# Optimization experiments

Measured on AMD Instinct MI355X. Metric: run time of the kernel, lower is better.

## Reference

```python
import jax, jax.numpy as jnp
import numpy as np

B, S, C = 4, 2048, 1024
H, D = 16, 64            # num_heads, head_size
N_STATE = H * D          # 1024
WINDOW = 256             # window_size (causal local window)
SCALE_INV = 1.0 / np.sqrt(D).astype(np.float32)  # sqrt_scale_inv**2 = 1/scale


def setup_inputs() -> dict:
    key = jax.random.key(0)
    ks = jax.random.split(key, 5)
    return {
        "x": jax.random.normal(ks[0], (B, S, C), dtype=jnp.float32),
        "W_qkv": jax.random.normal(ks[1], (3 * N_STATE, C), dtype=jnp.float32) * 0.02,
        "b_qkv": jax.random.normal(ks[2], (3 * N_STATE,), dtype=jnp.float32) * 0.02,
        "W_proj": jax.random.normal(ks[3], (C, N_STATE), dtype=jnp.float32) * 0.02,
        "b_proj": jax.random.normal(ks[4], (C,), dtype=jnp.float32) * 0.02,
    }


def reference(x, W_qkv, b_qkv, W_proj, b_proj):
    # fused QKV projection (channel_last Linear: y = x @ W.T + b)
    qkv = jnp.einsum("bsc,nc->bsn", x, W_qkv) + b_qkv        # [B,S,3*n_state]
    q, k, v = jnp.split(qkv, 3, axis=-1)

    def split_heads(t):  # [B,S,H*D] -> [B,H,S,D]
        return t.reshape(B, S, H, D).transpose(0, 2, 1, 3)

    q, k, v = split_heads(q), split_heads(k), split_heads(v)

    # scaled dot scores: matmul then multiply by 1/scale (scale = sqrt(head_size))
    scores = jnp.einsum("bhqd,bhkd->bhqk", q, k) * SCALE_INV  # [B,H,S,S]

    # window_ar mask: key j visible to query i iff 0 <= i - j < WINDOW
    i = jnp.arange(S)[:, None]
    j = jnp.arange(S)[None, :]
    allowed = (j <= i) & (i - j < WINDOW)                     # [S,S]
    scores = jnp.where(allowed, scores, -jnp.inf)

    attn = jax.nn.softmax(scores, axis=-1)                    # [B,H,S,S]
    ctx = jnp.einsum("bhqk,bhkd->bhqd", attn, v)              # [B,H,S,D]
    ctx = ctx.transpose(0, 2, 1, 3).reshape(B, S, N_STATE)    # merge heads

    out = jnp.einsum("bsn,cn->bsc", ctx, W_proj) + b_proj     # [B,S,C]
    return out
```

## Files before the change

kernel.cpp:

```cpp
#include <hip/hip_runtime.h>
#include <stdint.h>

#define S_LEN 2048
#define NH 16
#define HD 64
#define CDIM 1024
#define QKV_LD 3072
#define WIN 256

typedef __attribute__((ext_vector_type(8))) short bf16x8;
typedef __attribute__((ext_vector_type(4))) short bf16x4;
typedef __attribute__((ext_vector_type(4))) float f32x4;

__device__ __forceinline__ short f2bf(float f) {
  uint32_t u = __builtin_bit_cast(uint32_t, f);
  u += 0x7fffu + ((u >> 16) & 1u);
  return (short)(u >> 16);
}

__global__ void cvt_f32_bf16(const float* __restrict__ in, short* __restrict__ out, int n4) {
  int i = blockIdx.x * 256 + threadIdx.x;
  if (i >= n4) return;
  float4 v = ((const float4*)in)[i];
  bf16x4 o;
  o[0] = f2bf(v.x); o[1] = f2bf(v.y); o[2] = f2bf(v.z); o[3] = f2bf(v.w);
  ((bf16x4*)out)[i] = o;
}

__device__ __forceinline__ void gl_lds16(const short* g, short* lds) {
  __builtin_amdgcn_global_load_lds(
      (const __attribute__((address_space(1))) uint32_t*)(uintptr_t)g,
      (__attribute__((address_space(3))) uint32_t*)(uintptr_t)lds,
      16, 0, 0);
}

#define WAITVM(N) asm volatile("s_waitcnt vmcnt(" #N ")" ::: "memory")

template <int BF16OUT>
__global__ __launch_bounds__(512) void gemm_ring(
    const short* __restrict__ A, const short* __restrict__ Bt,
    const float* __restrict__ bias, void* __restrict__ Cout, int N)
{
  constexpr int K = 1024;
  constexpr int NSUB = 32;
  __shared__ __align__(16) short Asm[4][128 * 32];
  __shared__ __align__(16) short Bsm[4][256 * 32];
  const int tid = threadIdx.x, wave = tid >> 6, lane = tid & 63;
  const int wm = wave >> 2, wn = wave & 3;
  const int cl = lane & 15, g = lane >> 4;

  const int gx = gridDim.x;
  const int nwg = gx * gridDim.y;
  const int flat = blockIdx.y * gx + blockIdx.x;
  const int swzb = (flat & 7) * (nwg >> 3) + (flat >> 3);
  const int m0 = (swzb / gx) * 128;
  const int n0 = (swzb % gx) * 256;

  const int srow = tid >> 2;
  const int scol = (((tid & 3) ^ ((tid >> 3) & 3)) << 3);
  const short* Asrc  = A  + (size_t)(m0 + srow) * K + scol;
  const short* Bsrc0 = Bt + (size_t)(n0 + srow) * K + scol;
  const short* Bsrc1 = Bt + (size_t)(n0 + 128 + srow) * K + scol;
  const int ldso = tid * 8;

  auto stage = [&](int j) {
    const int st = j & 3;
    gl_lds16(Asrc  + j * 32, &Asm[st][ldso]);
    gl_lds16(Bsrc0 + j * 32, &Bsm[st][ldso]);
    gl_lds16(Bsrc1 + j * 32, &Bsm[st][4096 + ldso]);
  };

  const int rc = (g ^ ((cl >> 1) & 3)) << 3;
  const int arow = wm * 64 + cl;
  const int brow = wn * 64 + cl;

  f32x4 acc[4][4] = {};
  bf16x8 a0[4], b0[4], a1[4], b1[4];

  stage(0); stage(1); stage(2);
  WAITVM(3);
  __builtin_amdgcn_s_barrier();

#define READF(AA, BB, jj) { const int _s = (jj) & 3;                          \
  _Pragma("unroll") for (int i = 0; i < 4; i++)                               \
    AA[i] = *(const bf16x8*)&Asm[_s][(arow + i * 16) * 32 + rc];              \
  _Pragma("unroll") for (int n = 0; n < 4; n++)                               \
    BB[n] = *(const bf16x8*)&Bsm[_s][(brow + n * 16) * 32 + rc]; }

#define MFMA16(AA, BB)                                                        \
  __builtin_amdgcn_s_setprio(1);                                              \
  _Pragma("unroll") for (int i = 0; i < 4; i++)                               \
    _Pragma("unroll") for (int n = 0; n < 4; n++)                             \
      acc[i][n] = __builtin_amdgcn_mfma_f32_16x16x32_bf16(AA[i], BB[n], acc[i][n], 0, 0, 0); \
  __builtin_amdgcn_s_setprio(0);

  READF(a0, b0, 0);
  for (int j = 0; j < NSUB; j += 2) {
    READF(a1, b1, j + 1);
    if (j + 3 < NSUB) { stage(j + 3); WAITVM(3); } else { WAITVM(0); }
    __builtin_amdgcn_s_barrier();
    MFMA16(a0, b0);

    if (j + 2 < NSUB) READF(a0, b0, j + 2);
    if (j + 4 < NSUB) { stage(j + 4); WAITVM(3); } else { WAITVM(0); }
    __builtin_amdgcn_s_barrier();
    MFMA16(a1, b1);
  }
#undef READF
#undef MFMA16

#pragma unroll
  for (int n = 0; n < 4; n++) {
    const int col = n0 + wn * 64 + n * 16 + cl;
    const float bs = bias[col];
#pragma unroll
    for (int i = 0; i < 4; i++) {
      const int row = m0 + wm * 64 + i * 16 + g * 4;
#pragma unroll
      for (int e = 0; e < 4; e++) {
        const float v = acc[i][n][e] + bs;
        if (BF16OUT) ((short*)Cout)[(size_t)(row + e) * N + col] = f2bf(v);
        else         ((float*)Cout)[(size_t)(row + e) * N + col] = v;
      }
    }
  }
}

__global__ __launch_bounds__(256) void attn_win(
    const short* __restrict__ qkv, short* __restrict__ ctx)
{
  const int tid = threadIdx.x;
  const int wave = tid >> 6, lane = tid & 63;
  const int grp = blockIdx.x % 32;
  const int h = (blockIdx.x / 32) % NH;
  const int b = blockIdx.x / (32 * NH);
  const int qb = (grp * 4 + wave) * 16;

  const int cl = lane & 15;
  const int g  = lane >> 4;

  const size_t rowQ = (size_t)(b * S_LEN + qb + cl) * QKV_LD + h * HD;
  bf16x8 qf0 = *(const bf16x8*)&qkv[rowQ + g * 8];
  bf16x8 qf1 = *(const bf16x8*)&qkv[rowQ + 32 + g * 8];

  float m_run = -1e30f, l_run = 0.f;
  f32x4 acc[4] = {};
  const f32x4 zero = {};

  const int kstart = qb >= WIN ? qb - WIN : 0;
  const int q_glob = qb + cl;

  for (int k0 = kstart; k0 <= qb; k0 += 16) {
    const size_t rowK = (size_t)(b * S_LEN + k0 + cl) * QKV_LD + CDIM + h * HD;
    bf16x8 kf0 = *(const bf16x8*)&qkv[rowK + g * 8];
    bf16x8 kf1 = *(const bf16x8*)&qkv[rowK + 32 + g * 8];
    f32x4 st = __builtin_amdgcn_mfma_f32_16x16x32_bf16(kf0, qf0, zero, 0, 0, 0);
    st = __builtin_amdgcn_mfma_f32_16x16x32_bf16(kf1, qf1, st, 0, 0, 0);

    float s[4]; bool ok[4];
    float mt = -1e30f;
#pragma unroll
    for (int e = 0; e < 4; e++) {
      int key = k0 + 4 * g + e;
      ok[e] = (key <= q_glob) && (q_glob - key < WIN);
      s[e] = st[e] * 0.125f;
      if (ok[e]) mt = fmaxf(mt, s[e]);
    }
    mt = fmaxf(mt, __shfl_xor(mt, 16, 64));
    mt = fmaxf(mt, __shfl_xor(mt, 32, 64));
    float m_new = fmaxf(m_run, mt);
    float scale = __expf(m_run - m_new);
    float p[4]; float ls = 0.f;
#pragma unroll
    for (int e = 0; e < 4; e++) {
      p[e] = ok[e] ? __expf(s[e] - m_new) : 0.f;
      ls += p[e];
    }
    ls += __shfl_xor(ls, 16, 64);
    ls += __shfl_xor(ls, 32, 64);
    l_run = l_run * scale + ls;
    m_run = m_new;
#pragma unroll
    for (int c = 0; c < 4; c++) acc[c] *= scale;

    bf16x4 pf;
#pragma unroll
    for (int e = 0; e < 4; e++) pf[e] = f2bf(p[e]);

    const size_t rowV = (size_t)(b * S_LEN + k0 + 4 * g) * QKV_LD + 2 * CDIM + h * HD + cl;
#pragma unroll
    for (int c = 0; c < 4; c++) {
      bf16x4 vf;
#pragma unroll
      for (int e = 0; e < 4; e++)
        vf[e] = qkv[rowV + (size_t)e * QKV_LD + c * 16];
      acc[c] = __builtin_amdgcn_mfma_f32_16x16x16bf16_1k(vf, pf, acc[c], 0, 0, 0);
    }
  }

  const float inv_l = 1.f / l_run;
  const size_t rowO = (size_t)(b * S_LEN + qb + cl) * CDIM + h * HD;
#pragma unroll
  for (int c = 0; c < 4; c++)
#pragma unroll
    for (int j = 0; j < 4; j++)
      ctx[rowO + c * 16 + 4 * g + j] = f2bf(acc[c][j] * inv_l);
}

extern "C" void kernel_launch(void* const* d_in, const int* in_sizes, int n_in,
                              void* d_out, int out_size, void* d_ws, size_t ws_size,
                              hipStream_t stream) {
  const float* x      = (const float*)d_in[0];
  const float* W_qkv  = (const float*)d_in[1];
  const float* b_qkv  = (const float*)d_in[2];
  const float* W_proj = (const float*)d_in[3];
  const float* b_proj = (const float*)d_in[4];
  float* out = (float*)d_out;

  const int BS = 4 * S_LEN;
  char* ws = (char*)d_ws;
  short* qkv_bf = (short*)ws;
  short* x_bf   = (short*)(ws + (size_t)BS * QKV_LD * 2);
  short* wq_bf  = x_bf + (size_t)BS * CDIM;
  short* wp_bf  = wq_bf + (size_t)QKV_LD * CDIM;
  short* ctx_bf = wp_bf + (size_t)CDIM * CDIM;

  int n4 = BS * CDIM / 4;
  cvt_f32_bf16<<<(n4 + 255) / 256, 256, 0, stream>>>(x, x_bf, n4);
  n4 = QKV_LD * CDIM / 4;
  cvt_f32_bf16<<<(n4 + 255) / 256, 256, 0, stream>>>(W_qkv, wq_bf, n4);
  n4 = CDIM * CDIM / 4;
  cvt_f32_bf16<<<(n4 + 255) / 256, 256, 0, stream>>>(W_proj, wp_bf, n4);

  dim3 g1(QKV_LD / 256, BS / 128);
  gemm_ring<1><<<g1, 512, 0, stream>>>(x_bf, wq_bf, b_qkv, qkv_bf, QKV_LD);

  attn_win<<<4 * NH * 32, 256, 0, stream>>>(qkv_bf, ctx_bf);

  dim3 g2(CDIM / 256, BS / 128);
  gemm_ring<0><<<g2, 512, 0, stream>>>(ctx_bf, wp_bf, b_proj, out, CDIM);
}
```

Before: 249.9 us.

## Use larger 256x384 tile GEMM with 12 waves for the QKV projection

Adds a dedicated QKV GEMM kernel using 256x384 output tiles, 768 threads and one block per CU, giving exactly 256 workgroups, one per CU on mi355x. Each wave computes a 128x64 sub-tile and splits A reads into low and high halves so LDS reads and global-to-LDS staging interleave with MFMA work. The aim is more operand reuse per LDS load and no partial second wave of blocks. In exchange it uses much more LDS, has higher register pressure from 32 accumulators per lane, and relies on hand-tuned per-wave vmcnt waits.

```diff
diff --git a/kernel.cpp b/kernel.cpp
--- a/kernel.cpp
+++ b/kernel.cpp
@@ -35,6 +35,104 @@
 }
 
 #define WAITVM(N) asm volatile("s_waitcnt vmcnt(" #N ")" ::: "memory")
+
+__global__ __launch_bounds__(768, 1) void gemm_big(
+    const short* __restrict__ A, const short* __restrict__ Bt,
+    const float* __restrict__ bias, short* __restrict__ Cout)
+{
+  constexpr int K = 1024, NSUB = 32, NN = 3072;
+  __shared__ __align__(16) short Asm[4][256 * 32];
+  __shared__ __align__(16) short Bsm[4][384 * 32];
+  const int tid = threadIdx.x, wave = tid >> 6, lane = tid & 63;
+  const int wm = wave / 6, wn = wave % 6;
+  const int cl = lane & 15, g = lane >> 4;
+
+  const int bid = blockIdx.x;
+  const int swzb = (bid & 7) * 32 + (bid >> 3);
+  const int m0 = (swzb & 31) * 256;
+  const int n0 = (swzb >> 5) * 384;
+
+  const int srow = tid >> 2;
+  const int scc = (((tid & 3) ^ ((tid >> 3) & 3)) << 3);
+  const short* aS0 = A  + (size_t)(m0 + srow) * K + scc;
+  const short* aS1 = A  + (size_t)(m0 + 192 + srow) * K + scc;
+  const short* bS0 = Bt + (size_t)(n0 + srow) * K + scc;
+  const short* bS1 = Bt + (size_t)(n0 + 192 + srow) * K + scc;
+  const int d0 = tid * 8, d1 = 6144 + tid * 8;
+
+  auto stA = [&](int t) { const int s = t & 3;
+    gl_lds16(aS0 + t * 32, &Asm[s][d0]);
+    if (tid < 256) gl_lds16(aS1 + t * 32, &Asm[s][d1]);
+  };
+  auto stB = [&](int t) { const int s = t & 3;
+    gl_lds16(bS0 + t * 32, &Bsm[s][d0]);
+    gl_lds16(bS1 + t * 32, &Bsm[s][d1]);
+  };
+
+  const int rc = (g ^ ((cl >> 1) & 3)) << 3;
+  const int arow = wm * 128 + cl;
+  const int brow = wn * 64 + cl;
+
+  bf16x8 aLo[4], aHi[4], b0v[4], b1v[4];
+  f32x4 acc[8][4] = {};
+
+#define RD_ALO(jj) if ((jj) < NSUB) { const int _s = (jj) & 3;                \
+  _Pragma("unroll") for (int i = 0; i < 4; i++)                               \
+    aLo[i] = *(const bf16x8*)&Asm[_s][(arow + i * 16) * 32 + rc]; }
+#define RD_AHI(jj) { const int _s = (jj) & 3;                                 \
+  _Pragma("unroll") for (int i = 0; i < 4; i++)                               \
+    aHi[i] = *(const bf16x8*)&Asm[_s][(arow + 64 + i * 16) * 32 + rc]; }
+#define RD_B(BB, jj) if ((jj) < NSUB) { const int _s = (jj) & 3;              \
+  _Pragma("unroll") for (int n = 0; n < 4; n++)                               \
+    BB[n] = *(const bf16x8*)&Bsm[_s][(brow + n * 16) * 32 + rc]; }
+#define MFMAH(base, AA, BB)                                                   \
+  __builtin_amdgcn_s_setprio(1);                                              \
+  _Pragma("unroll") for (int i = 0; i < 4; i++)                               \
+    _Pragma("unroll") for (int n = 0; n < 4; n++)                             \
+      acc[(base) + i][n] = __builtin_amdgcn_mfma_f32_16x16x32_bf16(           \
+          AA[i], BB[n], acc[(base) + i][n], 0, 0, 0);                         \
+  __builtin_amdgcn_s_setprio(0);
+#define WAITG() { if (wave < 4) { WAITVM(6); } else { WAITVM(4); } }
+
+#define SUBP(jj, BC, BNx)                                                     \
+  RD_AHI(jj);                                                                 \
+  if ((jj) + 3 < NSUB) { stA((jj) + 3); WAITG(); } else { WAITVM(0); }        \
+  __builtin_amdgcn_s_barrier();                                               \
+  MFMAH(0, aLo, BC);                                                          \
+  RD_ALO((jj) + 1); RD_B(BNx, (jj) + 1);                                      \
+  if ((jj) + 3 < NSUB) { stB((jj) + 3); WAITG(); } else { WAITVM(0); }        \
+  __builtin_amdgcn_s_barrier();                                               \
+  MFMAH(4, aHi, BC);
+
+  stA(0); stB(0); stA(1); stB(1); stA(2); stB(2);
+  if (wave < 4) { WAITVM(8); } else { WAITVM(6); }
+  __builtin_amdgcn_s_barrier();
+  RD_ALO(0); RD_B(b0v, 0);
+
+  for (int j = 0; j < NSUB; j += 2) {
+    SUBP(j, b0v, b1v);
+    SUBP(j + 1, b1v, b0v);
+  }
+#undef RD_ALO
+#undef RD_AHI
+#undef RD_B
+#undef MFMAH
+#undef WAITG
+#undef SUBP
+
+#pragma unroll
+  for (int n = 0; n < 4; n++) {
+    const int col = n0 + wn * 64 + n * 16 + cl;
+    const float bs = bias[col];
+#pragma unroll
+    for (int i = 0; i < 8; i++) {
+      const int row = m0 + wm * 128 + i * 16 + g * 4;
+#pragma unroll
+      for (int e = 0; e < 4; e++)
+        Cout[(size_t)(row + e) * NN + col] = f2bf(acc[i][n][e] + bs);
+    }
+  }
+}
 
 template <int BF16OUT>
 __global__ __launch_bounds__(512) void gemm_ring(
@@ -58,7 +156,7 @@
 
   const int srow = tid >> 2;
   const int scol = (((tid & 3) ^ ((tid >> 3) & 3)) << 3);
-  const short* Asrc  = A  + (size_t)(m0 + srow) * K + scol;
+  const short* Asrc  = A + (size_t)(m0 + srow) * K + scol;
   const short* Bsrc0 = Bt + (size_t)(n0 + srow) * K + scol;
   const short* Bsrc1 = Bt + (size_t)(n0 + 128 + srow) * K + scol;
   const int ldso = tid * 8;
@@ -232,8 +330,7 @@
   n4 = CDIM * CDIM / 4;
   cvt_f32_bf16<<<(n4 + 255) / 256, 256, 0, stream>>>(W_proj, wp_bf, n4);
 
-  dim3 g1(QKV_LD / 256, BS / 128);
-  gemm_ring<1><<<g1, 512, 0, stream>>>(x_bf, wq_bf, b_qkv, qkv_bf, QKV_LD);
+  gemm_big<<<256, 768, 0, stream>>>(x_bf, wq_bf, b_qkv, qkv_bf);
 
   attn_win<<<4 * NH * 32, 256, 0, stream>>>(qkv_bf, ctx_bf);
 
```

Result: slower. 601.8 us (+140.9%).

## Replace QKV GEMM with 256x384-tile, 12-wave kernel sized to one wave of CUs

Applied to the files above, without the earlier changes.

Adds a dedicated QKV projection GEMM that uses 256x384 output tiles with 768 threads (12 waves, each computing 128x64). The grid is exactly 256 workgroups, matching the CU count, which removes the tail effect of the previous 768-block launch and raises arithmetic intensity per LDS load. A and B staging are split across the two half-steps, and explicit lgkmcnt waits and sched barriers are added around the MFMA phases. The cost is lower occupancy (one block per CU with large LDS and register use) and extra barriers per k-step, which may expose latency.

```diff
diff --git a/kernel.cpp b/kernel.cpp
--- a/kernel.cpp
+++ b/kernel.cpp
@@ -35,6 +35,110 @@
 }
 
 #define WAITVM(N) asm volatile("s_waitcnt vmcnt(" #N ")" ::: "memory")
+
+__global__ __launch_bounds__(768, 1) void gemm_qkv(
+    const short* __restrict__ A, const short* __restrict__ Bt,
+    const float* __restrict__ bias, short* __restrict__ Cout)
+{
+  constexpr int K = 1024, NSUB = 32, NN = 3072;
+  __shared__ __align__(16) short Asm[4][256 * 32];
+  __shared__ __align__(16) short Bsm[4][384 * 32];
+  const int tid = threadIdx.x, wave = tid >> 6, lane = tid & 63;
+  const int wm = wave / 6, wn = wave % 6;
+  const int cl = lane & 15, g = lane >> 4;
+
+  const int bid = blockIdx.x;
+  const int swzb = (bid & 7) * 32 + (bid >> 3);
+  const int m0 = (swzb & 31) * 256;
+  const int n0 = (swzb >> 5) * 384;
+
+  const int srow = tid >> 2;
+  const int scc = (((tid & 3) ^ ((tid >> 3) & 3)) << 3);
+  const short* aS0 = A  + (size_t)(m0 + srow) * K + scc;
+  const short* aS1 = A  + (size_t)(m0 + 128 + srow) * K + scc;
+  const short* bS0 = Bt + (size_t)(n0 + srow) * K + scc;
+  const short* bS1 = Bt + (size_t)(n0 + 192 + srow) * K + scc;
+  const int d8 = tid * 8;
+
+  auto stageA = [&](int t) { const int s = t & 3;
+    if (tid < 512) {
+      gl_lds16(aS0 + t * 32, &Asm[s][d8]);
+      gl_lds16(aS1 + t * 32, &Asm[s][4096 + d8]);
+    }
+  };
+  auto stageB = [&](int t) { const int s = t & 3;
+    gl_lds16(bS0 + t * 32, &Bsm[s][d8]);
+    gl_lds16(bS1 + t * 32, &Bsm[s][6144 + d8]);
+  };
+
+  const int rc = (g ^ ((cl >> 1) & 3)) << 3;
+  const int arow = wm * 128 + cl;
+  const int brow = wn * 64 + cl;
+
+  f32x4 acc[8][4] = {};
+
+  stageA(0); stageB(0); stageA(1); stageB(1); stageA(2); stageB(2);
+  if (wave < 8) { WAITVM(8); } else { WAITVM(4); }
+  __builtin_amdgcn_s_barrier();
+
+  for (int j = 0; j < NSUB; ++j) {
+    const int s = j & 3;
+    bf16x8 afr[4], bfr[4];
+
+#pragma unroll
+    for (int i = 0; i < 4; i++)
+      afr[i] = *(const bf16x8*)&Asm[s][(arow + i * 16) * 32 + rc];
+#pragma unroll
+    for (int n = 0; n < 4; n++)
+      bfr[n] = *(const bf16x8*)&Bsm[s][(brow + n * 16) * 32 + rc];
+    if (j + 3 < NSUB) stageA(j + 3);
+    __builtin_amdgcn_s_barrier();
+    asm volatile("s_waitcnt lgkmcnt(0)" ::: "memory");
+    __builtin_amdgcn_sched_barrier(0);
+    __builtin_amdgcn_s_setprio(1);
+#pragma unroll
+    for (int i = 0; i < 4; i++)
+#pragma unroll
+      for (int n = 0; n < 4; n++)
+        acc[i][n] = __builtin_amdgcn_mfma_f32_16x16x32_bf16(afr[i], bfr[n], acc[i][n], 0, 0, 0);
+    __builtin_amdgcn_s_setprio(0);
+    __builtin_amdgcn_s_barrier();
+
+#pragma unroll
+    for (int i = 0; i < 4; i++)
+      afr[i] = *(const bf16x8*)&Asm[s][(arow + 64 + i * 16) * 32 + rc];
+    if (j + 3 < NSUB) {
+      stageB(j + 3);
+      if (wave < 8) { WAITVM(8); } else { WAITVM(4); }
+    } else {
+      WAITVM(0);
+    }
+    __builtin_amdgcn_s_barrier();
+    asm volatile("s_waitcnt lgkmcnt(0)" ::: "memory");
+    __builtin_amdgcn_sched_barrier(0);
+    __builtin_amdgcn_s_setprio(1);
+#pragma unroll
+    for (int i = 0; i < 4; i++)
+#pragma unroll
+      for (int n = 0; n < 4; n++)
+        acc[4 + i][n] = __builtin_amdgcn_mfma_f32_16x16x32_bf16(afr[i], bfr[n], acc[4 + i][n], 0, 0, 0);
+    __builtin_amdgcn_s_setprio(0);
+    __builtin_amdgcn_s_barrier();
+  }
+
+#pragma unroll
+  for (int n = 0; n < 4; n++) {
+    const int col = n0 + wn * 64 + n * 16 + cl;
+    const float bs = bias[col];
+#pragma unroll
+    for (int i = 0; i < 8; i++) {
+      const int row = m0 + wm * 128 + i * 16 + g * 4;
+#pragma unroll
+      for (int e = 0; e < 4; e++)
+        Cout[(size_t)(row + e) * NN + col] = f2bf(acc[i][n][e] + bs);
+    }
+  }
+}
 
 template <int BF16OUT>
 __global__ __launch_bounds__(512) void gemm_ring(
@@ -58,7 +162,7 @@
 
   const int srow = tid >> 2;
   const int scol = (((tid & 3) ^ ((tid >> 3) & 3)) << 3);
-  const short* Asrc  = A  + (size_t)(m0 + srow) * K + scol;
+  const short* Asrc  = A + (size_t)(m0 + srow) * K + scol;
   const short* Bsrc0 = Bt + (size_t)(n0 + srow) * K + scol;
   const short* Bsrc1 = Bt + (size_t)(n0 + 128 + srow) * K + scol;
   const int ldso = tid * 8;
@@ -232,8 +336,7 @@
   n4 = CDIM * CDIM / 4;
   cvt_f32_bf16<<<(n4 + 255) / 256, 256, 0, stream>>>(W_proj, wp_bf, n4);
 
-  dim3 g1(QKV_LD / 256, BS / 128);
-  gemm_ring<1><<<g1, 512, 0, stream>>>(x_bf, wq_bf, b_qkv, qkv_bf, QKV_LD);
+  gemm_qkv<<<256, 768, 0, stream>>>(x_bf, wq_bf, b_qkv, qkv_bf);
 
   attn_win<<<4 * NH * 32, 256, 0, stream>>>(qkv_bf, ctx_bf);
 
```

New measurement: 271.4 us. 8.6% more time.

## Rewrite windowed attention with 32x32 MFMA tiles and XCD-aware block swizzle

Applied to the files above, without the earlier changes.

Replaces the 16-query-per-wave attention kernel with one where each wave handles 32 queries and 32 keys per step, using 32x32x16 bf16 MFMAs for both QK^T and PV. The P tile is repacked with cross-half lane shuffles so it can be fed straight into the PV MFMA. V loads are issued early with incrementing offsets, and blocks are remapped with a stride-8 swizzle. The aim is fewer loop iterations, fewer cross-lane reductions and more work per instruction, at the cost of more registers and wasted work on partially masked 32-key tiles.

```diff
diff --git a/kernel.cpp b/kernel.cpp
--- a/kernel.cpp
+++ b/kernel.cpp
@@ -11,11 +11,16 @@
 typedef __attribute__((ext_vector_type(8))) short bf16x8;
 typedef __attribute__((ext_vector_type(4))) short bf16x4;
 typedef __attribute__((ext_vector_type(4))) float f32x4;
+typedef __attribute__((ext_vector_type(16))) float f32x16;
+typedef __attribute__((ext_vector_type(4))) uint32_t u32x4;
 
 __device__ __forceinline__ short f2bf(float f) {
   uint32_t u = __builtin_bit_cast(uint32_t, f);
   u += 0x7fffu + ((u >> 16) & 1u);
   return (short)(u >> 16);
+}
+__device__ __forceinline__ uint32_t pk2(float lo, float hi) {
+  return ((uint32_t)(uint16_t)f2bf(hi) << 16) | (uint16_t)f2bf(lo);
 }
 
 __global__ void cvt_f32_bf16(const float* __restrict__ in, short* __restrict__ out, int n4) {
@@ -58,7 +63,7 @@
 
   const int srow = tid >> 2;
   const int scol = (((tid & 3) ^ ((tid >> 3) & 3)) << 3);
-  const short* Asrc  = A  + (size_t)(m0 + srow) * K + scol;
+  const short* Asrc  = A + (size_t)(m0 + srow) * K + scol;
   const short* Bsrc0 = Bt + (size_t)(n0 + srow) * K + scol;
   const short* Bsrc1 = Bt + (size_t)(n0 + 128 + srow) * K + scol;
   const int ldso = tid * 8;
@@ -126,85 +131,133 @@
   }
 }
 
-__global__ __launch_bounds__(256) void attn_win(
+__global__ __launch_bounds__(256) void attn_win32(
     const short* __restrict__ qkv, short* __restrict__ ctx)
 {
-  const int tid = threadIdx.x;
-  const int wave = tid >> 6, lane = tid & 63;
-  const int grp = blockIdx.x % 32;
-  const int h = (blockIdx.x / 32) % NH;
-  const int b = blockIdx.x / (32 * NH);
-  const int qb = (grp * 4 + wave) * 16;
-
-  const int cl = lane & 15;
-  const int g  = lane >> 4;
-
-  const size_t rowQ = (size_t)(b * S_LEN + qb + cl) * QKV_LD + h * HD;
-  bf16x8 qf0 = *(const bf16x8*)&qkv[rowQ + g * 8];
-  bf16x8 qf1 = *(const bf16x8*)&qkv[rowQ + 32 + g * 8];
+  const int lane = threadIdx.x & 63;
+  const int wave = threadIdx.x >> 6;
+  const int c32 = lane & 31, h32 = lane >> 5;
+
+  const int bid = blockIdx.x;
+  const int swz = (bid & 7) * 128 + (bid >> 3);
+  const int grp = swz & 15;
+  const int h = (swz >> 4) & 15;
+  const int b = swz >> 8;
+  const int qb = (grp * 4 + wave) * 32;
+  const int q = qb + c32;
+
+  const short* Qb = qkv + (size_t)(b * S_LEN) * QKV_LD + h * HD;
+  const short* Kb = Qb + CDIM;
+  const short* Vb = Qb + 2 * CDIM;
+
+  bf16x8 qf[4];
+  {
+    const short* qrow = Qb + (size_t)(qb + c32) * QKV_LD + 8 * h32;
+#pragma unroll
+    for (int t = 0; t < 4; t++) qf[t] = *(const bf16x8*)(qrow + 16 * t);
+  }
+
+  const int kstart = qb >= WIN ? qb - WIN : 0;
+  uint32_t offV[8];
+#pragma unroll
+  for (int e = 0; e < 8; e++)
+    offV[e] = (uint32_t)(kstart + 8 * h32 + e) * QKV_LD + c32;
 
   float m_run = -1e30f, l_run = 0.f;
-  f32x4 acc[4] = {};
-  const f32x4 zero = {};
-
-  const int kstart = qb >= WIN ? qb - WIN : 0;
-  const int q_glob = qb + cl;
-
-  for (int k0 = kstart; k0 <= qb; k0 += 16) {
-    const size_t rowK = (size_t)(b * S_LEN + k0 + cl) * QKV_LD + CDIM + h * HD;
-    bf16x8 kf0 = *(const bf16x8*)&qkv[rowK + g * 8];
-    bf16x8 kf1 = *(const bf16x8*)&qkv[rowK + 32 + g * 8];
-    f32x4 st = __builtin_amdgcn_mfma_f32_16x16x32_bf16(kf0, qf0, zero, 0, 0, 0);
-    st = __builtin_amdgcn_mfma_f32_16x16x32_bf16(kf1, qf1, st, 0, 0, 0);
-
-    float s[4]; bool ok[4];
+  f32x16 accLo = {}, accHi = {};
+
+  for (int k0 = kstart; k0 <= qb; k0 += 32) {
+    f32x16 st = {};
+    {
+      const short* krow = Kb + (size_t)(k0 + c32) * QKV_LD + 8 * h32;
+#pragma unroll
+      for (int t = 0; t < 4; t++) {
+        bf16x8 kf = *(const bf16x8*)(krow + 16 * t);
+        st = __builtin_amdgcn_mfma_f32_32x32x16_bf16(kf, qf[t], st, 0, 0, 0);
+      }
+    }
+
+    short vL0[8], vH0[8], vL1[8], vH1[8];
+#pragma unroll
+    for (int e = 0; e < 8; e++) {
+      vL0[e] = Vb[offV[e]]; vH0[e] = Vb[offV[e] + 32];
+      offV[e] += 16 * QKV_LD;
+    }
+#pragma unroll
+    for (int e = 0; e < 8; e++) {
+      vL1[e] = Vb[offV[e]]; vH1[e] = Vb[offV[e] + 32];
+      offV[e] += 16 * QKV_LD;
+    }
+
+    const int dq = q - k0;
+    float p[16];
     float mt = -1e30f;
 #pragma unroll
-    for (int e = 0; e < 4; e++) {
-      int key = k0 + 4 * g + e;
-      ok[e] = (key <= q_glob) && (q_glob - key < WIN);
-      s[e] = st[e] * 0.125f;
-      if (ok[e]) mt = fmaxf(mt, s[e]);
-    }
-    mt = fmaxf(mt, __shfl_xor(mt, 16, 64));
+    for (int r = 0; r < 16; r++) {
+      const int kk = (r & 3) + 8 * (r >> 2) + 4 * h32;
+      const bool ok = (uint32_t)(dq - kk) < (uint32_t)WIN;
+      p[r] = ok ? st[r] * 0.125f : -1e30f;
+      mt = fmaxf(mt, p[r]);
+    }
     mt = fmaxf(mt, __shfl_xor(mt, 32, 64));
-    float m_new = fmaxf(m_run, mt);
-    float scale = __expf(m_run - m_new);
-    float p[4]; float ls = 0.f;
-#pragma unroll
-    for (int e = 0; e < 4; e++) {
-      p[e] = ok[e] ? __expf(s[e] - m_new) : 0.f;
-      ls += p[e];
-    }
-    ls += __shfl_xor(ls, 16, 64);
+    const float m_new = fmaxf(m_run, mt);
+    const float scale = __expf(m_run - m_new);
+    float ls = 0.f;
+#pragma unroll
+    for (int r = 0; r < 16; r++) {
+      p[r] = (p[r] > -1e29f) ? __expf(p[r] - m_new) : 0.f;
+      ls += p[r];
+    }
     ls += __shfl_xor(ls, 32, 64);
     l_run = l_run * scale + ls;
     m_run = m_new;
 #pragma unroll
-    for (int c = 0; c < 4; c++) acc[c] *= scale;
-
-    bf16x4 pf;
-#pragma unroll
-    for (int e = 0; e < 4; e++) pf[e] = f2bf(p[e]);
-
-    const size_t rowV = (size_t)(b * S_LEN + k0 + 4 * g) * QKV_LD + 2 * CDIM + h * HD + cl;
-#pragma unroll
-    for (int c = 0; c < 4; c++) {
-      bf16x4 vf;
-#pragma unroll
-      for (int e = 0; e < 4; e++)
-        vf[e] = qkv[rowV + (size_t)e * QKV_LD + c * 16];
-      acc[c] = __builtin_amdgcn_mfma_f32_16x16x16bf16_1k(vf, pf, acc[c], 0, 0, 0);
+    for (int i = 0; i < 16; i++) { accLo[i] *= scale; accHi[i] *= scale; }
+
+    uint32_t w[8];
+#pragma unroll
+    for (int u = 0; u < 4; u++) {
+      w[2 * u]     = pk2(p[4 * u],     p[4 * u + 1]);
+      w[2 * u + 1] = pk2(p[4 * u + 2], p[4 * u + 3]);
+    }
+
+#pragma unroll
+    for (int t = 0; t < 2; t++) {
+      const uint32_t a0 = w[4 * t], a1 = w[4 * t + 1];
+      const uint32_t b0 = w[4 * t + 2], b1 = w[4 * t + 3];
+      const uint32_t snd0 = h32 ? a0 : b0, snd1 = h32 ? a1 : b1;
+      const uint32_t x0 = (uint32_t)__shfl_xor((int)snd0, 32, 64);
+      const uint32_t x1 = (uint32_t)__shfl_xor((int)snd1, 32, 64);
+      u32x4 bw;
+      bw[0] = h32 ? x0 : a0;
+      bw[1] = h32 ? x1 : a1;
+      bw[2] = h32 ? b0 : x0;
+      bw[3] = h32 ? b1 : x1;
+      const bf16x8 pf = __builtin_bit_cast(bf16x8, bw);
+
+      bf16x8 vlo, vhi;
+#pragma unroll
+      for (int e = 0; e < 8; e++) {
+        vlo[e] = t == 0 ? vL0[e] : vL1[e];
+        vhi[e] = t == 0 ? vH0[e] : vH1[e];
+      }
+      accLo = __builtin_amdgcn_mfma_f32_32x32x16_bf16(vlo, pf, accLo, 0, 0, 0);
+      accHi = __builtin_amdgcn_mfma_f32_32x32x16_bf16(vhi, pf, accHi, 0, 0, 0);
     }
   }
 
   const float inv_l = 1.f / l_run;
-  const size_t rowO = (size_t)(b * S_LEN + qb + cl) * CDIM + h * HD;
-#pragma unroll
-  for (int c = 0; c < 4; c++)
-#pragma unroll
-    for (int j = 0; j < 4; j++)
-      ctx[rowO + c * 16 + 4 * g + j] = f2bf(acc[c][j] * inv_l);
+  short* orow = ctx + (size_t)(b * S_LEN + q) * CDIM + h * HD;
+#pragma unroll
+  for (int u = 0; u < 4; u++) {
+    bf16x4 o;
+#pragma unroll
+    for (int j = 0; j < 4; j++) o[j] = f2bf(accLo[4 * u + j] * inv_l);
+    *(bf16x4*)(orow + 8 * u + 4 * h32) = o;
+#pragma unroll
+    for (int j = 0; j < 4; j++) o[j] = f2bf(accHi[4 * u + j] * inv_l);
+    *(bf16x4*)(orow + 32 + 8 * u + 4 * h32) = o;
+  }
 }
 
 extern "C" void kernel_launch(void* const* d_in, const int* in_sizes, int n_in,
@@ -235,7 +288,7 @@
   dim3 g1(QKV_LD / 256, BS / 128);
   gemm_ring<1><<<g1, 512, 0, stream>>>(x_bf, wq_bf, b_qkv, qkv_bf, QKV_LD);
 
-  attn_win<<<4 * NH * 32, 256, 0, stream>>>(qkv_bf, ctx_bf);
+  attn_win32<<<1024, 256, 0, stream>>>(qkv_bf, ctx_bf);
 
   dim3 g2(CDIM / 256, BS / 128);
   gemm_ring<0><<<g2, 512, 0, stream>>>(ctx_bf, wp_bf, b_proj, out, CDIM);
```

New measurement: 233.7 us. 6.5% less time.
